# Optimization experiments

Hardware: AMD Instinct MI355X
Metric: run time of the kernel (lower is better)

The kernel has to match this reference:

```python
import jax, jax.numpy as jnp
import numpy as np

# Sizes: B graphs of N nodes each, K nearest neighbours, D=feat_dim=nhid, C=pos_dim
B, N, K, D, C = 4, 1024, 128, 32, 2
L = 3                     # number of EGNN conv layers
E_IN = 2 * D + 1          # edge MLP input: feats_i | feats_j | rel_dist (edge_dim=0, fourier=0)
E_H = 2 * E_IN            # edge MLP hidden


def _lin(key, fan_in, fan_out):
    kw, kb = jax.random.split(key)
    w = jax.random.normal(kw, (fan_in, fan_out), jnp.float32) / np.sqrt(fan_in)
    b = jax.random.normal(kb, (fan_out,), jnp.float32) * 0.01
    return w, b


def _stack(key, fan_in, fan_out):
    ws, bs = zip(*[_lin(k, fan_in, fan_out) for k in jax.random.split(key, L)])
    return jnp.stack(ws), jnp.stack(bs)


def setup_inputs() -> dict:
    key = jax.random.key(0)
    ks = jax.random.split(key, 10)
    feat_ = jax.random.normal(ks[0], (B * N, D), jnp.float32)
    coor_ = jax.random.normal(ks[1], (B * N, C), jnp.float32)
    batch = jnp.full((B,), N, dtype=jnp.int32)   # per-graph node counts (equal-size graphs)
    embed_w, embed_b = _lin(ks[2], D, D)         # embed: Linear(feat_dim, nhid)
    e1_w, e1_b = _stack(ks[3], E_IN, E_H)        # edge MLP
    e2_w, e2_b = _stack(ks[4], E_H, D)           # -> m_dim = nhid
    gate_w, gate_b = _stack(ks[5], D, 1)         # soft_edges gate
    c1_w, c1_b = _stack(ks[6], D, 4 * D)         # coors MLP
    c2_w, c2_b = _stack(ks[7], 4 * D, 1)
    n1_w, n1_b = _stack(ks[8], 2 * D, 2 * D)     # node MLP
    n2_w, n2_b = _stack(ks[9], 2 * D, D)
    coors_scale = jnp.full((L, 1), 1e-2, jnp.float32)  # CoorsNorm scale (init 1e-2)
    return dict(feat_=feat_, coor_=coor_, batch=batch, embed_w=embed_w, embed_b=embed_b,
                e1_w=e1_w, e1_b=e1_b, e2_w=e2_w, e2_b=e2_b, gate_w=gate_w, gate_b=gate_b,
                c1_w=c1_w, c1_b=c1_b, c2_w=c2_w, c2_b=c2_b, n1_w=n1_w, n1_b=n1_b,
                n2_w=n2_w, n2_b=n2_b, coors_scale=coors_scale)


def _lrelu(x):
    return jax.nn.leaky_relu(x, 0.1)


def _gather(x, idx):
    # x: [B, n, d], idx: [B, n, k] -> [B, n, k, d]
    return jax.vmap(lambda xb, ib: xb[ib])(x, idx)


def _egnn_layer(feats, coors, p):
    (e1_w, e1_b, e2_w, e2_b, gate_w, gate_b, c1_w, c1_b, c2_w, c2_b,
     n1_w, n1_b, n2_w, n2_b, scale) = p
    # pairwise squared distances; k smallest (self included, valid_radius=inf)
    diff = coors[:, :, None, :] - coors[:, None, :, :]      # [B,n,n,C]
    dist = jnp.sum(diff * diff, axis=-1)                    # [B,n,n]
    neg_d, idx = jax.lax.top_k(-dist, K)                    # k nearest
    rel_dist = -neg_d[..., None]                            # [B,n,K,1]
    rel_coors = coors[:, :, None, :] - _gather(coors, idx)  # [B,n,K,C]
    feats_j = _gather(feats, idx)                           # [B,n,K,D]
    feats_i = jnp.broadcast_to(feats[:, :, None, :], feats_j.shape)
    edge_in = jnp.concatenate([feats_i, feats_j, rel_dist], axis=-1)  # [B,n,K,E_IN]
    # edge MLP: Lin -> act -> Lin -> act ; soft edge gate
    m = _lrelu(_lrelu(edge_in @ e1_w + e1_b) @ e2_w + e2_b)            # [B,n,K,D]
    m = m * jax.nn.sigmoid(m @ gate_w + gate_b)
    # coordinate update: coors_mlp -> scalar weights; CoorsNorm on rel coords
    cw = (_lrelu(m @ c1_w + c1_b) @ c2_w + c2_b)[..., 0]               # [B,n,K]
    norm = jnp.maximum(jnp.linalg.norm(rel_coors, axis=-1, keepdims=True), 1e-8)
    rel_n = rel_coors / norm * scale
    coors_out = jnp.einsum('bik,bikc->bic', cw, rel_n) + coors
    # feature update: sum-pool messages, node MLP with residual
    m_i = jnp.sum(m, axis=2)                                           # [B,n,D]
    node_in = jnp.concatenate([feats, m_i], axis=-1)
    feats_out = _lrelu(node_in @ n1_w + n1_b) @ n2_w + n2_b + feats
    return feats_out, coors_out


def reference(feat_, coor_, batch, embed_w, embed_b, e1_w, e1_b, e2_w, e2_b,
              gate_w, gate_b, c1_w, c1_b, c2_w, c2_b, n1_w, n1_b, n2_w, n2_b,
              coors_scale):
    # embed MLP (dropout is identity at p=0 / eval), then batch equal-size graphs
    feats = _lrelu(feat_ @ embed_w + embed_b).reshape(B, N, D)
    coors = coor_.reshape(B, N, C)
    for l in range(L):
        p = (e1_w[l], e1_b[l], e2_w[l], e2_b[l], gate_w[l], gate_b[l],
             c1_w[l], c1_b[l], c2_w[l], c2_b[l], n1_w[l], n1_b[l],
             n2_w[l], n2_b[l], coors_scale[l])
        feats, coors = _egnn_layer(feats, coors, p)
    return feats.reshape(B * N, D)
```

## Files before the change

kernel.cpp:

```cpp
#include <hip/hip_runtime.h>
#include <hip/hip_bf16.h>
#include <math.h>

#define BB 4
#define NN 1024
#define KK 128
#define DD 32
#define LL 3
#define EH 130
#define EHP 132

typedef float f32x4 __attribute__((ext_vector_type(4)));
typedef short s16x8 __attribute__((ext_vector_type(8)));

__device__ __forceinline__ float lrelu(float x) { return fmaxf(x, 0.1f * x); }

__device__ __forceinline__ unsigned pk2(float a, float b) {
    __hip_bfloat162 h = __float22bfloat162_rn(float2{a, b});
    return *(unsigned*)&h;
}
__device__ __forceinline__ unsigned short bf16_hu(float v) {
    return (unsigned short)((__float_as_uint(v) + 0x8000u) >> 16);
}
__device__ __forceinline__ unsigned short bf16_rne(float v) {
    unsigned u = __float_as_uint(v);
    return (unsigned short)((u + 0x7fffu + ((u >> 16) & 1u)) >> 16);
}

__device__ __forceinline__ void knn_select(const float2* __restrict__ cbp, int i, int lane,
                                           int* __restrict__ nb) {
    const float2 ci = cbp[i];
    unsigned k[16];
#pragma unroll
    for (int s = 0; s < 16; s++) {
        float2 cj = cbp[lane + 64 * s];
        float dx = ci.x - cj.x, dy = ci.y - cj.y;
        float d = __fadd_rn(__fmul_rn(dx, dx), __fmul_rn(dy, dy));
        k[s] = __float_as_uint(d);
    }
    unsigned P = 0;
    for (int bpos = 30; bpos >= 0; bpos--) {
        const unsigned X = P | (1u << bpos);
        unsigned c = 0;
#pragma unroll
        for (int s = 0; s < 16; s++)
            c += (unsigned)__popcll(__ballot(k[s] < X));
        if (c < (unsigned)KK) P = X;
    }
    const unsigned dstar = P;
    const unsigned long long below = (1ull << lane) - 1ull;
    unsigned run = 0;
#pragma unroll
    for (int s = 0; s < 16; s++) {
        unsigned long long m = __ballot(k[s] < dstar);
        if (k[s] < dstar) nb[run + (unsigned)__popcll(m & below)] = lane + 64 * s;
        run += (unsigned)__popcll(m);
    }
    const int need = KK - (int)run;
    unsigned tie = 0;
    for (int s = 0; s < 16 && (int)tie < need; s++) {
        unsigned long long m = __ballot(k[s] == dstar);
        if (k[s] == dstar) {
            unsigned r = tie + (unsigned)__popcll(m & below);
            if ((int)r < need) nb[run + r] = lane + 64 * s;
        }
        tie += (unsigned)__popcll(m);
    }
}

__global__ __launch_bounds__(128) void prep_kernel(
    const float* __restrict__ feat, const float* __restrict__ coor,
    const float* __restrict__ ew, const float* __restrict__ eb,
    float* __restrict__ fout,
    const float* __restrict__ e1w0, const float* __restrict__ e1b0,
    float* __restrict__ HI, float* __restrict__ HJ,
    int* __restrict__ nbr,
    const float* __restrict__ e2w, const float* __restrict__ c1w,
    unsigned short* __restrict__ e2f, unsigned short* __restrict__ c1f) {
    const int bid = blockIdx.x;
    const int t = threadIdx.x;
    if (bid < 2048) {
        __shared__ float sfe[2][DD];
        const int n0 = bid * 2;
        if (t < 64) {
            const int nl = t >> 5, o = t & 31;
            const float* f = feat + (size_t)(n0 + nl) * DD;
            float a = eb[o];
#pragma unroll
            for (int k = 0; k < DD; k++) a = fmaf(f[k], ew[k * DD + o], a);
            a = lrelu(a);
            fout[(size_t)(n0 + nl) * DD + o] = a;
            sfe[nl][o] = a;
        }
        __syncthreads();
        for (int idx = t; idx < 2 * EHP; idx += 128) {
            const int nl = idx / EHP, o = idx - nl * EHP;
            const size_t off = (size_t)(n0 + nl) * EHP + o;
            if (o >= EH) { HI[off] = 0.f; HJ[off] = 0.f; continue; }
            const float* fl = sfe[nl];
            float aa = e1b0[o], cc = 0.f;
#pragma unroll
            for (int k = 0; k < DD; k++) aa = fmaf(fl[k], e1w0[k * EH + o], aa);
#pragma unroll
            for (int k = 0; k < DD; k++) cc = fmaf(fl[k], e1w0[(DD + k) * EH + o], cc);
            HI[off] = aa;
            HJ[off] = cc;
        }
    } else if (bid < 4096) {
        const int node = (bid - 2048) * 2 + (t >> 6);
        const int b = node >> 10, i = node & (NN - 1);
        knn_select((const float2*)coor + (size_t)b * NN, i, t & 63,
                   nbr + (size_t)node * KK);
    } else {
        for (int u = (bid - 4096) * 128 + t; u < 2 * LL * 4096; u += 96 * 128) {
            if (u < LL * 4096) {
                int jj = u & 7, la = (u >> 3) & 63, nt = (u >> 9) & 1, c = (u >> 10) & 3, l = u >> 12;
                int k = 32 * c + (la >> 4) * 8 + jj;
                int n = nt * 16 + (la & 15);
                e2f[u] = bf16_rne(e2w[(size_t)l * EH * DD + k * DD + n]);
            } else {
                int v = u - LL * 4096;
                int jj = v & 7, la = (v >> 3) & 63, nt = (v >> 9) & 7, l = v >> 12;
                int k = (la >> 4) * 8 + jj;
                int n = nt * 16 + (la & 15);
                c1f[v] = bf16_rne(c1w[(size_t)l * DD * 128 + k * 128 + n]);
            }
        }
    }
}

__global__ __launch_bounds__(256) void knnpre_kernel(
    const float* __restrict__ coors, int* __restrict__ nbr,
    const float* __restrict__ feats, const float* __restrict__ e1w, const float* __restrict__ e1b,
    float* __restrict__ HI, float* __restrict__ HJ) {
    const int KNNB = BB * NN / 4;
    if (blockIdx.x >= KNNB) {
        int t = (int)(blockIdx.x - KNNB) * 256 + threadIdx.x;
        if (t >= BB * NN * EHP) return;
        int n = t / EHP, o = t % EHP;
        if (o >= EH) { HI[t] = 0.f; HJ[t] = 0.f; return; }
        const float* f = feats + n * DD;
        float a = e1b[o], c = 0.f;
#pragma unroll
        for (int k = 0; k < DD; k++) a = fmaf(f[k], e1w[k * EH + o], a);
#pragma unroll
        for (int k = 0; k < DD; k++) c = fmaf(f[k], e1w[(DD + k) * EH + o], c);
        HI[t] = a;
        HJ[t] = c;
        return;
    }
    const int node = (int)blockIdx.x * 4 + (threadIdx.x >> 6);
    const int b = node >> 10, i = node & (NN - 1);
    knn_select((const float2*)coors + (size_t)b * NN, i, threadIdx.x & 63,
               nbr + (size_t)node * KK);
}

__global__ __launch_bounds__(128) void layer_kernel(
    const float* __restrict__ feats_in, const float* __restrict__ coors_in,
    const int*   __restrict__ nbr,
    const float* __restrict__ HI, const float* __restrict__ HJ,
    const float* __restrict__ w65,
    const float* __restrict__ e2w,
    const float* __restrict__ e2b,
    const unsigned short* __restrict__ e2f,
    const unsigned short* __restrict__ c1f,
    const float* __restrict__ gw, const float* __restrict__ gb,
    const float* __restrict__ c1b, const float* __restrict__ c2w, const float* __restrict__ c2b,
    const float* __restrict__ n1w, const float* __restrict__ n1b,
    const float* __restrict__ n2w, const float* __restrict__ n2b,
    const float* __restrict__ scale,
    float* __restrict__ feats_out, float* __restrict__ coors_out) {
    const int node = blockIdx.x;
    const int b = node >> 10;
    const int t = threadIdx.x;
    const int lane = t & 63, wid = t >> 6;
    const int ln = lane & 15, q = lane >> 4;
    const int rowbase = wid * 64;

    __shared__ __align__(16) float shi[EHP];
    __shared__ __align__(16) float sw65[EHP];
    __shared__ __align__(16) unsigned short smA[2 * 64 * 32];
    __shared__ float sx0[128], sx1[128], su[128], sv[128];
    __shared__ float sgw[DD], se2b[DD], sfi[DD];
    __shared__ float sc1b[128], sc2w[128];
    __shared__ float redm[2][DD], redc[2][2];
    __shared__ float sni[2 * DD], shd[2 * DD];

    for (int u = t; u < EHP; u += 128) {
        shi[u] = HI[(size_t)node * EHP + u];
        sw65[u] = (u < EH) ? w65[u] : 0.f;
    }
    if (t < DD) { sfi[t] = feats_in[node * DD + t]; sgw[t] = gw[t]; se2b[t] = e2b[t]; }
    sc1b[t] = c1b[t];
    sc2w[t] = c2w[t];
    __syncthreads();

    const float cix = coors_in[node * 2], ciy = coors_in[node * 2 + 1];
    const int j = nbr[(size_t)node * KK + t];
    const float2 cj = *(const float2*)(coors_in + ((size_t)(b * NN) + j) * 2);
    const float dx = cix - cj.x, dy = ciy - cj.y;
    const float rd = __fadd_rn(__fmul_rn(dx, dx), __fmul_rn(dy, dy));
    const float nrm = fmaxf(sqrtf(rd), 1e-8f);
    const float s = scale[0] / nrm;
    su[t] = dx * s;
    sv[t] = dy * s;

    {
        const float2 hjt = *(const float2*)(HJ + ((size_t)(b * NN) + j) * EHP + 128);
        sx0[t] = lrelu(shi[128] + hjt.x + rd * sw65[128]);
        sx1[t] = lrelu(shi[129] + hjt.y + rd * sw65[129]);
    }

    const float* hjb[4];
    float rdR[4];
#pragma unroll
    for (int mt = 0; mt < 4; mt++) {
        int jR = __shfl(j, mt * 16 + ln, 64);
        rdR[mt] = __shfl(rd, mt * 16 + ln, 64);
        hjb[mt] = HJ + ((size_t)(b * NN) + jR) * EHP;
    }

    const float4* shi4 = (const float4*)shi;
    const float4* sw4  = (const float4*)sw65;

    const f32x4 zz = {0.f, 0.f, 0.f, 0.f};
    f32x4 accA[4][2];
#pragma unroll
    for (int mt = 0; mt < 4; mt++) { accA[mt][0] = zz; accA[mt][1] = zz; }

    float4 ha[4], hbv[4];
#pragma unroll
    for (int mt = 0; mt < 4; mt++) {
        const float4* hjp = (const float4*)(hjb[mt] + q * 8);
        ha[mt] = hjp[0];
        hbv[mt] = hjp[1];
    }

#pragma unroll 1
    for (int c = 0; c < 4; c++) {
        s16x8 b0 = *(const s16x8*)(e2f + ((c * 2 + 0) * 64 + lane) * 8);
        s16x8 b1 = *(const s16x8*)(e2f + ((c * 2 + 1) * 64 + lane) * 8);
        float4 nha[4], nhb[4];
        if (c < 3) {
#pragma unroll
            for (int mt = 0; mt < 4; mt++) {
                const float4* hjp = (const float4*)(hjb[mt] + (c + 1) * 32 + q * 8);
                nha[mt] = hjp[0];
                nhb[mt] = hjp[1];
            }
        }
        const int kb = c * 8 + q * 2;
        const float4 hi0 = shi4[kb], hi1 = shi4[kb + 1];
        const float4 wv0 = sw4[kb],  wv1 = sw4[kb + 1];
#pragma unroll
        for (int mt = 0; mt < 4; mt++) {
            const float r = rdR[mt];
            union { s16x8 v; unsigned u[4]; } A;
            A.u[0] = pk2(lrelu(hi0.x + ha[mt].x + r * wv0.x), lrelu(hi0.y + ha[mt].y + r * wv0.y));
            A.u[1] = pk2(lrelu(hi0.z + ha[mt].z + r * wv0.z), lrelu(hi0.w + ha[mt].w + r * wv0.w));
            A.u[2] = pk2(lrelu(hi1.x + hbv[mt].x + r * wv1.x), lrelu(hi1.y + hbv[mt].y + r * wv1.y));
            A.u[3] = pk2(lrelu(hi1.z + hbv[mt].z + r * wv1.z), lrelu(hi1.w + hbv[mt].w + r * wv1.w));
            accA[mt][0] = __builtin_amdgcn_mfma_f32_16x16x32_bf16(A.v, b0, accA[mt][0], 0, 0, 0);
            accA[mt][1] = __builtin_amdgcn_mfma_f32_16x16x32_bf16(A.v, b1, accA[mt][1], 0, 0, 0);
        }
#pragma unroll
        for (int mt = 0; mt < 4; mt++) { ha[mt] = nha[mt]; hbv[mt] = nhb[mt]; }
    }

#pragma unroll
    for (int nt = 0; nt < 2; nt++) {
        const int col = nt * 16 + ln;
        const float w128 = e2w[128 * DD + col];
        const float w129 = e2w[129 * DD + col];
        const float bv = se2b[col];
#pragma unroll
        for (int mt = 0; mt < 4; mt++)
#pragma unroll
            for (int r = 0; r < 4; r++) {
                const int row = rowbase + mt * 16 + q * 4 + r;
                accA[mt][nt][r] = lrelu(accA[mt][nt][r] + bv + sx0[row] * w128 + sx1[row] * w129);
            }
    }

    const float gbv = gb[0];
#pragma unroll
    for (int mt = 0; mt < 4; mt++) {
        float p[4];
#pragma unroll
        for (int r = 0; r < 4; r++)
            p[r] = accA[mt][0][r] * sgw[ln] + accA[mt][1][r] * sgw[16 + ln];
#pragma unroll
        for (int off = 1; off <= 8; off <<= 1)
#pragma unroll
            for (int r = 0; r < 4; r++) p[r] += __shfl_xor(p[r], off);
#pragma unroll
        for (int r = 0; r < 4; r++) {
            const float g = 1.f / (1.f + __expf(-(p[r] + gbv)));
            accA[mt][0][r] *= g;
            accA[mt][1][r] *= g;
        }
    }

    float mi0 = 0.f, mi1 = 0.f;
#pragma unroll
    for (int mt = 0; mt < 4; mt++)
#pragma unroll
        for (int r = 0; r < 4; r++) { mi0 += accA[mt][0][r]; mi1 += accA[mt][1][r]; }
    mi0 += __shfl_xor(mi0, 16); mi0 += __shfl_xor(mi0, 32);
    mi1 += __shfl_xor(mi1, 16); mi1 += __shfl_xor(mi1, 32);
    if (lane < 16) { redm[wid][lane] = mi0; redm[wid][16 + lane] = mi1; }

    unsigned short* smw = smA + wid * (64 * 32);
#pragma unroll
    for (int mt = 0; mt < 4; mt++)
#pragma unroll
        for (int nt = 0; nt < 2; nt++)
#pragma unroll
            for (int r = 0; r < 4; r++) {
                const int prow = (r << 4) | (4 * mt + q);
                smw[prow * 32 + nt * 16 + ln] = bf16_hu(accA[mt][nt][r]);
            }

    s16x8 a4[4];
#pragma unroll
    for (int mt = 0; mt < 4; mt++) {
        const int prow = ((ln & 3) << 4) | (4 * mt + (ln >> 2));
        a4[mt] = *(const s16x8*)(smw + prow * 32 + q * 8);
    }

    float cacc[4][4];
#pragma unroll
    for (int mt = 0; mt < 4; mt++)
#pragma unroll
        for (int r = 0; r < 4; r++) cacc[mt][r] = 0.f;

#pragma unroll 1
    for (int g = 0; g < 4; g++) {
        s16x8 bc0 = *(const s16x8*)(c1f + ((2 * g + 0) * 64 + lane) * 8);
        s16x8 bc1 = *(const s16x8*)(c1f + ((2 * g + 1) * 64 + lane) * 8);
        f32x4 c20[4], c21[4];
#pragma unroll
        for (int mt = 0; mt < 4; mt++) {
            c20[mt] = __builtin_amdgcn_mfma_f32_16x16x32_bf16(a4[mt], bc0, zz, 0, 0, 0);
            c21[mt] = __builtin_amdgcn_mfma_f32_16x16x32_bf16(a4[mt], bc1, zz, 0, 0, 0);
        }
#pragma unroll
        for (int h = 0; h < 2; h++) {
            const int col = (2 * g + h) * 16 + ln;
            const float c1bv = sc1b[col], c2wv = sc2w[col];
#pragma unroll
            for (int mt = 0; mt < 4; mt++)
#pragma unroll
                for (int r = 0; r < 4; r++) {
                    const float v = (h ? c21[mt][r] : c20[mt][r]) + c1bv;
                    cacc[mt][r] = fmaf(lrelu(v), c2wv, cacc[mt][r]);
                }
        }
    }
#pragma unroll
    for (int off = 1; off <= 8; off <<= 1)
#pragma unroll
        for (int mt = 0; mt < 4; mt++)
#pragma unroll
            for (int r = 0; r < 4; r++) cacc[mt][r] += __shfl_xor(cacc[mt][r], off);

    const float c2bv = c2b[0];
    float vxp = 0.f, vyp = 0.f;
    if (ln == 0) {
#pragma unroll
        for (int mt = 0; mt < 4; mt++)
#pragma unroll
            for (int r = 0; r < 4; r++) {
                const int row = rowbase + mt * 16 + q * 4 + r;
                const float cw = cacc[mt][r] + c2bv;
                vxp = fmaf(cw, su[row], vxp);
                vyp = fmaf(cw, sv[row], vyp);
            }
    }
    vxp += __shfl_xor(vxp, 16); vxp += __shfl_xor(vxp, 32);
    vyp += __shfl_xor(vyp, 16); vyp += __shfl_xor(vyp, 32);
    if (lane == 0) { redc[wid][0] = vxp; redc[wid][1] = vyp; }

    __syncthreads();
    if (t < DD) {
        sni[t] = sfi[t];
        sni[DD + t] = redm[0][t] + redm[1][t];
    }
    __syncthreads();
    if (t < 2 * DD) {
        float a = n1b[t];
#pragma unroll
        for (int k = 0; k < 2 * DD; k++) a = fmaf(sni[k], n1w[k * 2 * DD + t], a);
        shd[t] = lrelu(a);
    }
    __syncthreads();
    if (t < DD) {
        float a = n2b[t];
#pragma unroll
        for (int o = 0; o < 2 * DD; o++) a = fmaf(shd[o], n2w[o * DD + t], a);
        feats_out[node * DD + t] = a + sfi[t];
    }
    if (t == 0) {
        coors_out[node * 2] = cix + redc[0][0] + redc[1][0];
        coors_out[node * 2 + 1] = ciy + redc[0][1] + redc[1][1];
    }
}

extern "C" void kernel_launch(void* const* d_in, const int* in_sizes, int n_in,
                              void* d_out, int out_size, void* d_ws, size_t ws_size,
                              hipStream_t stream) {
    const float* feat_   = (const float*)d_in[0];
    const float* coor_   = (const float*)d_in[1];
    const float* embed_w = (const float*)d_in[3];
    const float* embed_b = (const float*)d_in[4];
    const float* e1_w    = (const float*)d_in[5];
    const float* e1_b    = (const float*)d_in[6];
    const float* e2_w    = (const float*)d_in[7];
    const float* e2_b    = (const float*)d_in[8];
    const float* gate_w  = (const float*)d_in[9];
    const float* gate_b  = (const float*)d_in[10];
    const float* c1_w    = (const float*)d_in[11];
    const float* c1_b    = (const float*)d_in[12];
    const float* c2_w    = (const float*)d_in[13];
    const float* c2_b    = (const float*)d_in[14];
    const float* n1_w    = (const float*)d_in[15];
    const float* n1_b    = (const float*)d_in[16];
    const float* n2_w    = (const float*)d_in[17];
    const float* n2_b    = (const float*)d_in[18];
    const float* cscale  = (const float*)d_in[19];

    float* ws = (float*)d_ws;
    float* fa   = ws;   ws += BB * NN * DD;
    float* fb   = ws;   ws += BB * NN * DD;
    float* ca   = ws;   ws += BB * NN * 2;
    float* cb2  = ws;   ws += BB * NN * 2;
    float* HIa  = ws;   ws += BB * NN * EHP;
    float* HJa  = ws;   ws += BB * NN * EHP;
    unsigned short* e2f = (unsigned short*)ws;
    unsigned short* c1f = e2f + LL * 4096;
    int* nbr = (int*)(c1f + LL * 4096);

    prep_kernel<<<4096 + 96, 128, 0, stream>>>(feat_, coor_, embed_w, embed_b, fa,
                                               e1_w, e1_b, HIa, HJa, nbr,
                                               e2_w, c1_w, e2f, c1f);

    const int KNNB = BB * NN / 4;
    const int PREB = (BB * NN * EHP + 255) / 256;
    const float* fin = fa;
    const float* cin = coor_;
    float* fouts[LL] = {fb, fa, (float*)d_out};
    float* couts[LL] = {ca, cb2, ca};

    for (int l = 0; l < LL; l++) {
        if (l > 0)
            knnpre_kernel<<<KNNB + PREB, 256, 0, stream>>>(
                cin, nbr, fin, e1_w + (size_t)l * 65 * EH, e1_b + (size_t)l * EH, HIa, HJa);
        layer_kernel<<<BB * NN, 128, 0, stream>>>(
            fin, cin, nbr, HIa, HJa,
            e1_w + ((size_t)l * 65 + 64) * EH,
            e2_w + (size_t)l * EH * DD,
            e2_b + (size_t)l * DD,
            e2f + (size_t)l * 4096,
            c1f + (size_t)l * 4096,
            gate_w + (size_t)l * DD,
            gate_b + l,
            c1_b + (size_t)l * 128,
            c2_w + (size_t)l * 128,
            c2_b + l,
            n1_w + (size_t)l * 64 * 64,
            n1_b + (size_t)l * 64,
            n2_w + (size_t)l * 64 * 32,
            n2_b + (size_t)l * DD,
            cscale + l,
            fouts[l], couts[l]);
        fin = fouts[l];
        cin = couts[l];
    }
}
```

Baseline: 324.8 us.

## Use four waves per node and fold edge-MLP tail into extra MFMA

The per-node layer kernel now runs four waves (256 threads), each handling 32 neighbour rows instead of 64. Neighbour indices and distances are staged through shared memory instead of shuffles. The scalar epilogue that added the bias and the last two hidden columns of the second edge-MLP matrix is replaced by a fifth padded bf16 MFMA k-chunk. That chunk packs those two weight rows and the bias into the preformatted weight buffer. This aims to raise occupancy and latency hiding and remove per-element scalar work, at the cost of an extra block sync, bf16 rounding of the bias and tail terms, and idle threads in the serial tail.

After: 318.4 us. 1.02x faster.

```diff
diff --git a/kernel.cpp b/kernel.cpp
--- a/kernel.cpp
+++ b/kernel.cpp
@@ -75,7 +75,8 @@
     const float* __restrict__ e1w0, const float* __restrict__ e1b0,
     float* __restrict__ HI, float* __restrict__ HJ,
     int* __restrict__ nbr,
-    const float* __restrict__ e2w, const float* __restrict__ c1w,
+    const float* __restrict__ e2w, const float* __restrict__ e2b,
+    const float* __restrict__ c1w,
     unsigned short* __restrict__ e2f, unsigned short* __restrict__ c1f) {
     const int bid = blockIdx.x;
     const int t = threadIdx.x;
@@ -112,14 +113,26 @@
         knn_select((const float2*)coor + (size_t)b * NN, i, t & 63,
                    nbr + (size_t)node * KK);
     } else {
-        for (int u = (bid - 4096) * 128 + t; u < 2 * LL * 4096; u += 96 * 128) {
-            if (u < LL * 4096) {
-                int jj = u & 7, la = (u >> 3) & 63, nt = (u >> 9) & 1, c = (u >> 10) & 3, l = u >> 12;
-                int k = 32 * c + (la >> 4) * 8 + jj;
+        const int TOT_E2 = LL * 5120;
+        const int TOT = TOT_E2 + LL * 4096;
+        for (int u = (bid - 4096) * 128 + t; u < TOT; u += 96 * 128) {
+            if (u < TOT_E2) {
+                int l = u / 5120, v = u - l * 5120;
+                int jj = v & 7, la = (v >> 3) & 63, nt = (v >> 9) & 1, c = v >> 10;
                 int n = nt * 16 + (la & 15);
-                e2f[u] = bf16_rne(e2w[(size_t)l * EH * DD + k * DD + n]);
+                float val;
+                if (c < 4) {
+                    int k = 32 * c + (la >> 4) * 8 + jj;
+                    val = e2w[(size_t)l * EH * DD + k * DD + n];
+                } else {
+                    int ks = (la >> 4) * 8 + jj;
+                    val = (ks == 0) ? e2w[((size_t)l * EH + 128) * DD + n]
+                        : (ks == 1) ? e2w[((size_t)l * EH + 129) * DD + n]
+                        : (ks == 2) ? e2b[(size_t)l * DD + n] : 0.f;
+                }
+                e2f[u] = bf16_rne(val);
             } else {
-                int v = u - LL * 4096;
+                int v = u - TOT_E2;
                 int jj = v & 7, la = (v >> 3) & 63, nt = (v >> 9) & 7, l = v >> 12;
                 int k = (la >> 4) * 8 + jj;
                 int n = nt * 16 + (la & 15);
@@ -155,13 +168,11 @@
                nbr + (size_t)node * KK);
 }
 
-__global__ __launch_bounds__(128) void layer_kernel(
+__global__ __launch_bounds__(256) void layer_kernel(
     const float* __restrict__ feats_in, const float* __restrict__ coors_in,
     const int*   __restrict__ nbr,
     const float* __restrict__ HI, const float* __restrict__ HJ,
     const float* __restrict__ w65,
-    const float* __restrict__ e2w,
-    const float* __restrict__ e2b,
     const unsigned short* __restrict__ e2f,
     const unsigned short* __restrict__ c1f,
     const float* __restrict__ gw, const float* __restrict__ gb,
@@ -175,62 +186,63 @@
     const int t = threadIdx.x;
     const int lane = t & 63, wid = t >> 6;
     const int ln = lane & 15, q = lane >> 4;
-    const int rowbase = wid * 64;
+    const int rowbase = wid * 32;
 
     __shared__ __align__(16) float shi[EHP];
     __shared__ __align__(16) float sw65[EHP];
-    __shared__ __align__(16) unsigned short smA[2 * 64 * 32];
-    __shared__ float sx0[128], sx1[128], su[128], sv[128];
-    __shared__ float sgw[DD], se2b[DD], sfi[DD];
+    __shared__ __align__(16) unsigned short smA[4 * 32 * 32];
+    __shared__ float sx0[128], sx1[128], su[128], sv[128], srd[128];
+    __shared__ int snb[128];
+    __shared__ float sgw[DD], sfi[DD];
     __shared__ float sc1b[128], sc2w[128];
-    __shared__ float redm[2][DD], redc[2][2];
+    __shared__ float redm[4][DD], redc[4][2];
     __shared__ float sni[2 * DD], shd[2 * DD];
 
-    for (int u = t; u < EHP; u += 128) {
+    for (int u = t; u < EHP; u += 256) {
         shi[u] = HI[(size_t)node * EHP + u];
         sw65[u] = (u < EH) ? w65[u] : 0.f;
     }
-    if (t < DD) { sfi[t] = feats_in[node * DD + t]; sgw[t] = gw[t]; se2b[t] = e2b[t]; }
-    sc1b[t] = c1b[t];
-    sc2w[t] = c2w[t];
+    if (t < DD) { sfi[t] = feats_in[node * DD + t]; sgw[t] = gw[t]; }
+    if (t >= 128) { sc1b[t - 128] = c1b[t - 128]; sc2w[t - 128] = c2w[t - 128]; }
     __syncthreads();
 
     const float cix = coors_in[node * 2], ciy = coors_in[node * 2 + 1];
-    const int j = nbr[(size_t)node * KK + t];
-    const float2 cj = *(const float2*)(coors_in + ((size_t)(b * NN) + j) * 2);
-    const float dx = cix - cj.x, dy = ciy - cj.y;
-    const float rd = __fadd_rn(__fmul_rn(dx, dx), __fmul_rn(dy, dy));
-    const float nrm = fmaxf(sqrtf(rd), 1e-8f);
-    const float s = scale[0] / nrm;
-    su[t] = dx * s;
-    sv[t] = dy * s;
-
-    {
+    if (t < 128) {
+        const int j = nbr[(size_t)node * KK + t];
+        snb[t] = j;
+        const float2 cj = *(const float2*)(coors_in + ((size_t)(b * NN) + j) * 2);
+        const float dx = cix - cj.x, dy = ciy - cj.y;
+        const float rd = __fadd_rn(__fmul_rn(dx, dx), __fmul_rn(dy, dy));
+        srd[t] = rd;
+        const float nrm = fmaxf(sqrtf(rd), 1e-8f);
+        const float s = scale[0] / nrm;
+        su[t] = dx * s;
+        sv[t] = dy * s;
         const float2 hjt = *(const float2*)(HJ + ((size_t)(b * NN) + j) * EHP + 128);
         sx0[t] = lrelu(shi[128] + hjt.x + rd * sw65[128]);
         sx1[t] = lrelu(shi[129] + hjt.y + rd * sw65[129]);
     }
-
-    const float* hjb[4];
-    float rdR[4];
-#pragma unroll
-    for (int mt = 0; mt < 4; mt++) {
-        int jR = __shfl(j, mt * 16 + ln, 64);
-        rdR[mt] = __shfl(rd, mt * 16 + ln, 64);
-        hjb[mt] = HJ + ((size_t)(b * NN) + jR) * EHP;
+    __syncthreads();
+
+    float rdR[2];
+    const float* hjb[2];
+#pragma unroll
+    for (int mt = 0; mt < 2; mt++) {
+        const int row = rowbase + mt * 16 + ln;
+        rdR[mt] = srd[row];
+        hjb[mt] = HJ + ((size_t)(b * NN) + snb[row]) * EHP;
     }
 
     const float4* shi4 = (const float4*)shi;
     const float4* sw4  = (const float4*)sw65;
 
     const f32x4 zz = {0.f, 0.f, 0.f, 0.f};
-    f32x4 accA[4][2];
-#pragma unroll
-    for (int mt = 0; mt < 4; mt++) { accA[mt][0] = zz; accA[mt][1] = zz; }
-
-    float4 ha[4], hbv[4];
-#pragma unroll
-    for (int mt = 0; mt < 4; mt++) {
+    f32x4 accA[2][2];
+    accA[0][0] = zz; accA[0][1] = zz; accA[1][0] = zz; accA[1][1] = zz;
+
+    float4 ha[2], hbv[2];
+#pragma unroll
+    for (int mt = 0; mt < 2; mt++) {
         const float4* hjp = (const float4*)(hjb[mt] + q * 8);
         ha[mt] = hjp[0];
         hbv[mt] = hjp[1];
@@ -240,10 +252,10 @@
     for (int c = 0; c < 4; c++) {
         s16x8 b0 = *(const s16x8*)(e2f + ((c * 2 + 0) * 64 + lane) * 8);
         s16x8 b1 = *(const s16x8*)(e2f + ((c * 2 + 1) * 64 + lane) * 8);
-        float4 nha[4], nhb[4];
+        float4 nha[2], nhb[2];
         if (c < 3) {
 #pragma unroll
-            for (int mt = 0; mt < 4; mt++) {
+            for (int mt = 0; mt < 2; mt++) {
                 const float4* hjp = (const float4*)(hjb[mt] + (c + 1) * 32 + q * 8);
                 nha[mt] = hjp[0];
                 nhb[mt] = hjp[1];
@@ -253,7 +265,7 @@
         const float4 hi0 = shi4[kb], hi1 = shi4[kb + 1];
         const float4 wv0 = sw4[kb],  wv1 = sw4[kb + 1];
 #pragma unroll
-        for (int mt = 0; mt < 4; mt++) {
+        for (int mt = 0; mt < 2; mt++) {
             const float r = rdR[mt];
             union { s16x8 v; unsigned u[4]; } A;
             A.u[0] = pk2(lrelu(hi0.x + ha[mt].x + r * wv0.x), lrelu(hi0.y + ha[mt].y + r * wv0.y));
@@ -264,27 +276,37 @@
             accA[mt][1] = __builtin_amdgcn_mfma_f32_16x16x32_bf16(A.v, b1, accA[mt][1], 0, 0, 0);
         }
 #pragma unroll
-        for (int mt = 0; mt < 4; mt++) { ha[mt] = nha[mt]; hbv[mt] = nhb[mt]; }
-    }
-
-#pragma unroll
-    for (int nt = 0; nt < 2; nt++) {
-        const int col = nt * 16 + ln;
-        const float w128 = e2w[128 * DD + col];
-        const float w129 = e2w[129 * DD + col];
-        const float bv = se2b[col];
-#pragma unroll
-        for (int mt = 0; mt < 4; mt++)
-#pragma unroll
-            for (int r = 0; r < 4; r++) {
-                const int row = rowbase + mt * 16 + q * 4 + r;
-                accA[mt][nt][r] = lrelu(accA[mt][nt][r] + bv + sx0[row] * w128 + sx1[row] * w129);
-            }
-    }
+        for (int mt = 0; mt < 2; mt++) { ha[mt] = nha[mt]; hbv[mt] = nhb[mt]; }
+    }
+
+    {
+        s16x8 b40 = *(const s16x8*)(e2f + ((4 * 2 + 0) * 64 + lane) * 8);
+        s16x8 b41 = *(const s16x8*)(e2f + ((4 * 2 + 1) * 64 + lane) * 8);
+#pragma unroll
+        for (int mt = 0; mt < 2; mt++) {
+            const int row = rowbase + mt * 16 + ln;
+            union { s16x8 v; unsigned u[4]; } A;
+            const unsigned p0 = pk2(sx0[row], sx1[row]);
+            A.u[0] = (q == 0) ? p0 : 0u;
+            A.u[1] = (q == 0) ? 0x00003f80u : 0u;
+            A.u[2] = 0u;
+            A.u[3] = 0u;
+            accA[mt][0] = __builtin_amdgcn_mfma_f32_16x16x32_bf16(A.v, b40, accA[mt][0], 0, 0, 0);
+            accA[mt][1] = __builtin_amdgcn_mfma_f32_16x16x32_bf16(A.v, b41, accA[mt][1], 0, 0, 0);
+        }
+    }
+
+#pragma unroll
+    for (int mt = 0; mt < 2; mt++)
+#pragma unroll
+        for (int nt = 0; nt < 2; nt++)
+#pragma unroll
+            for (int r = 0; r < 4; r++)
+                accA[mt][nt][r] = lrelu(accA[mt][nt][r]);
 
     const float gbv = gb[0];
 #pragma unroll
-    for (int mt = 0; mt < 4; mt++) {
+    for (int mt = 0; mt < 2; mt++) {
         float p[4];
 #pragma unroll
         for (int r = 0; r < 4; r++)
@@ -303,34 +325,34 @@
 
     float mi0 = 0.f, mi1 = 0.f;
 #pragma unroll
-    for (int mt = 0; mt < 4; mt++)
+    for (int mt = 0; mt < 2; mt++)
 #pragma unroll
         for (int r = 0; r < 4; r++) { mi0 += accA[mt][0][r]; mi1 += accA[mt][1][r]; }
     mi0 += __shfl_xor(mi0, 16); mi0 += __shfl_xor(mi0, 32);
     mi1 += __shfl_xor(mi1, 16); mi1 += __shfl_xor(mi1, 32);
     if (lane < 16) { redm[wid][lane] = mi0; redm[wid][16 + lane] = mi1; }
 
-    unsigned short* smw = smA + wid * (64 * 32);
-#pragma unroll
-    for (int mt = 0; mt < 4; mt++)
+    unsigned short* smw = smA + wid * (32 * 32);
+#pragma unroll
+    for (int mt = 0; mt < 2; mt++)
 #pragma unroll
         for (int nt = 0; nt < 2; nt++)
 #pragma unroll
             for (int r = 0; r < 4; r++) {
-                const int prow = (r << 4) | (4 * mt + q);
+                const int prow = (r << 3) | (4 * mt + q);
                 smw[prow * 32 + nt * 16 + ln] = bf16_hu(accA[mt][nt][r]);
             }
 
-    s16x8 a4[4];
-#pragma unroll
-    for (int mt = 0; mt < 4; mt++) {
-        const int prow = ((ln & 3) << 4) | (4 * mt + (ln >> 2));
+    s16x8 a4[2];
+#pragma unroll
+    for (int mt = 0; mt < 2; mt++) {
+        const int prow = ((ln & 3) << 3) | (4 * mt + (ln >> 2));
         a4[mt] = *(const s16x8*)(smw + prow * 32 + q * 8);
     }
 
-    float cacc[4][4];
-#pragma unroll
-    for (int mt = 0; mt < 4; mt++)
+    float cacc[2][4];
+#pragma unroll
+    for (int mt = 0; mt < 2; mt++)
 #pragma unroll
         for (int r = 0; r < 4; r++) cacc[mt][r] = 0.f;
 
@@ -338,9 +360,9 @@
     for (int g = 0; g < 4; g++) {
         s16x8 bc0 = *(const s16x8*)(c1f + ((2 * g + 0) * 64 + lane) * 8);
         s16x8 bc1 = *(const s16x8*)(c1f + ((2 * g + 1) * 64 + lane) * 8);
-        f32x4 c20[4], c21[4];
-#pragma unroll
-        for (int mt = 0; mt < 4; mt++) {
+        f32x4 c20[2], c21[2];
+#pragma unroll
+        for (int mt = 0; mt < 2; mt++) {
             c20[mt] = __builtin_amdgcn_mfma_f32_16x16x32_bf16(a4[mt], bc0, zz, 0, 0, 0);
             c21[mt] = __builtin_amdgcn_mfma_f32_16x16x32_bf16(a4[mt], bc1, zz, 0, 0, 0);
         }
@@ -349,7 +371,7 @@
             const int col = (2 * g + h) * 16 + ln;
             const float c1bv = sc1b[col], c2wv = sc2w[col];
 #pragma unroll
-            for (int mt = 0; mt < 4; mt++)
+            for (int mt = 0; mt < 2; mt++)
 #pragma unroll
                 for (int r = 0; r < 4; r++) {
                     const float v = (h ? c21[mt][r] : c20[mt][r]) + c1bv;
@@ -360,7 +382,7 @@
 #pragma unroll
     for (int off = 1; off <= 8; off <<= 1)
 #pragma unroll
-        for (int mt = 0; mt < 4; mt++)
+        for (int mt = 0; mt < 2; mt++)
 #pragma unroll
             for (int r = 0; r < 4; r++) cacc[mt][r] += __shfl_xor(cacc[mt][r], off);
 
@@ -368,7 +390,7 @@
     float vxp = 0.f, vyp = 0.f;
     if (ln == 0) {
 #pragma unroll
-        for (int mt = 0; mt < 4; mt++)
+        for (int mt = 0; mt < 2; mt++)
 #pragma unroll
             for (int r = 0; r < 4; r++) {
                 const int row = rowbase + mt * 16 + q * 4 + r;
@@ -384,7 +406,7 @@
     __syncthreads();
     if (t < DD) {
         sni[t] = sfi[t];
-        sni[DD + t] = redm[0][t] + redm[1][t];
+        sni[DD + t] = redm[0][t] + redm[1][t] + redm[2][t] + redm[3][t];
     }
     __syncthreads();
     if (t < 2 * DD) {
@@ -401,8 +423,8 @@
         feats_out[node * DD + t] = a + sfi[t];
     }
     if (t == 0) {
-        coors_out[node * 2] = cix + redc[0][0] + redc[1][0];
-        coors_out[node * 2 + 1] = ciy + redc[0][1] + redc[1][1];
+        coors_out[node * 2]     = cix + redc[0][0] + redc[1][0] + redc[2][0] + redc[3][0];
+        coors_out[node * 2 + 1] = ciy + redc[0][1] + redc[1][1] + redc[2][1] + redc[3][1];
     }
 }
 
@@ -437,12 +459,12 @@
     float* HIa  = ws;   ws += BB * NN * EHP;
     float* HJa  = ws;   ws += BB * NN * EHP;
     unsigned short* e2f = (unsigned short*)ws;
-    unsigned short* c1f = e2f + LL * 4096;
+    unsigned short* c1f = e2f + LL * 5120;
     int* nbr = (int*)(c1f + LL * 4096);
 
     prep_kernel<<<4096 + 96, 128, 0, stream>>>(feat_, coor_, embed_w, embed_b, fa,
                                                e1_w, e1_b, HIa, HJa, nbr,
-                                               e2_w, c1_w, e2f, c1f);
+                                               e2_w, e2_b, c1_w, e2f, c1f);
 
     const int KNNB = BB * NN / 4;
     const int PREB = (BB * NN * EHP + 255) / 256;
@@ -455,12 +477,10 @@
         if (l > 0)
             knnpre_kernel<<<KNNB + PREB, 256, 0, stream>>>(
                 cin, nbr, fin, e1_w + (size_t)l * 65 * EH, e1_b + (size_t)l * EH, HIa, HJa);
-        layer_kernel<<<BB * NN, 128, 0, stream>>>(
+        layer_kernel<<<BB * NN, 256, 0, stream>>>(
             fin, cin, nbr, HIa, HJa,
             e1_w + ((size_t)l * 65 + 64) * EH,
-            e2_w + (size_t)l * EH * DD,
-            e2_b + (size_t)l * DD,
-            e2f + (size_t)l * 4096,
+            e2f + (size_t)l * 5120,
             c1f + (size_t)l * 4096,
             gate_w + (size_t)l * DD,
             gate_b + l,
```
